# Kernel optimization log

Measured on AMD Instinct MI355X. Metric: run time of the kernel, lower is better.

## Reference

```python
import jax, jax.numpy as jnp
import numpy as np

D_NODE, D_PAIR, H = 512, 128, 16
HD = D_NODE // H  # head_dim = 32
B, N = 2, 1024


def _layernorm(x, gamma, beta, eps=1e-5):
    mu = jnp.mean(x, axis=-1, keepdims=True)
    var = jnp.var(x, axis=-1, keepdims=True)
    return (x - mu) * jax.lax.rsqrt(var + eps) * gamma + beta


def setup_inputs() -> dict:
    key = jax.random.key(0)
    ks = jax.random.split(key, 16)
    sc = 0.02
    inp = {
        's': jax.random.normal(ks[0], (B, N, D_NODE), jnp.float32),
        'z': jax.random.normal(ks[1], (B, N, N, D_PAIR), jnp.float32),
        'key_mask': jax.random.randint(ks[2], (B, N), 0, 2).astype(bool),
        'Wq': jax.random.normal(ks[3], (D_NODE, D_NODE), jnp.float32) * sc,
        'bq': jnp.zeros((D_NODE,), jnp.float32),
        'Wk': jax.random.normal(ks[4], (D_NODE, D_NODE), jnp.float32) * sc,
        'bk': jnp.zeros((D_NODE,), jnp.float32),
        'Wv': jax.random.normal(ks[5], (D_NODE, D_NODE), jnp.float32) * sc,
        'bv': jnp.zeros((D_NODE,), jnp.float32),
        'Wb': jax.random.normal(ks[6], (D_PAIR, H), jnp.float32) * sc,
        'bb': jnp.zeros((H,), jnp.float32),
        'Wg': jax.random.normal(ks[7], (D_NODE, D_NODE), jnp.float32) * sc,
        'bg': jnp.zeros((D_NODE,), jnp.float32),
        'Wo': jax.random.normal(ks[8], (D_NODE, D_NODE), jnp.float32) * sc,
        'bo': jnp.zeros((D_NODE,), jnp.float32),
        'gamma': jnp.ones((D_NODE,), jnp.float32),
        'beta': jnp.zeros((D_NODE,), jnp.float32),
    }
    return inp


def reference(s, z, key_mask, Wq, bq, Wk, bk, Wv, bv, Wb, bb, Wg, bg, Wo, bo, gamma, beta):
    b, n, _ = s.shape
    sn = _layernorm(s, gamma, beta)
    q = (sn @ Wq + bq).reshape(b, n, H, HD)
    k = (sn @ Wk + bk).reshape(b, n, H, HD)
    v = (sn @ Wv + bv).reshape(b, n, H, HD)
    # scores: [B, N(query), N(key), H]
    scores = jnp.einsum('bnhd,bmhd->bnmh', q, k) / np.sqrt(HD).astype(np.float32)
    scores = scores + (z @ Wb + bb)  # additive pair bias
    # mask keys (dim 2); True = masked out
    scores = jnp.where(key_mask[:, None, :, None], -jnp.inf, scores)
    attn = jax.nn.softmax(scores, axis=2)
    attn = jnp.nan_to_num(attn, nan=0.0)
    out = jnp.einsum('bnmh,bmhd->bnhd', attn, v).reshape(b, n, D_NODE)
    gate = jax.nn.sigmoid(sn @ Wg + bg)
    return gate * (out @ Wo + bo)
```

## Files before the change

### kernel.cpp

```cpp
#include <hip/hip_runtime.h>
#include <hip/hip_fp16.h>

typedef __attribute__((ext_vector_type(8))) _Float16 f16x8;
typedef __attribute__((ext_vector_type(8))) unsigned short u16x8;
typedef __attribute__((ext_vector_type(4))) float f32x4;

#define DEV __device__ __forceinline__

DEV unsigned short f2h(float f) {
  _Float16 h = (_Float16)f;
  return __builtin_bit_cast(unsigned short, h);
}
DEV float h2f(unsigned short u) {
  return (float)__builtin_bit_cast(_Float16, u);
}
DEV unsigned pk(float lo, float hi) {
  return (unsigned)f2h(lo) | ((unsigned)f2h(hi) << 16);
}

__global__ __launch_bounds__(256) void k_mask(const unsigned* __restrict__ raw,
                                              int* __restrict__ canon) {
  __shared__ int s_gt1, s_f32;
  int t = threadIdx.x;
  if (t == 0) { s_gt1 = 0; s_f32 = 0; }
  __syncthreads();
  int gt1 = 0, fv = 0;
  for (int i = t; i < 512; i += 256) {
    unsigned v = raw[i];
    if (v == 0x3F800000u) fv = 1;
    else if (v > 1u) gt1 = 1;
  }
  if (gt1) s_gt1 = 1;
  if (fv)  s_f32 = 1;
  __syncthreads();
  int mode = s_gt1 ? 1 : (s_f32 ? 2 : 0);
  for (int i = t; i < 2048; i += 256) {
    int v;
    if (mode == 1)      v = ((const unsigned char*)raw)[i] ? 1 : 0;
    else if (mode == 2) v = (((const float*)raw)[i] != 0.f) ? 1 : 0;
    else                v = raw[i] ? 1 : 0;
    canon[i] = v;
  }
}

__global__ __launch_bounds__(64) void k_ln(const float* __restrict__ s,
                                           const float* __restrict__ gamma,
                                           const float* __restrict__ beta,
                                           unsigned short* __restrict__ sn) {
  int row = blockIdx.x, l = threadIdx.x;
  const float* sr = s + (size_t)row * 512 + l * 8;
  float4 x0 = *(const float4*)sr, x1 = *(const float4*)(sr + 4);
  float sum = x0.x + x0.y + x0.z + x0.w + x1.x + x1.y + x1.z + x1.w;
  float sq  = x0.x*x0.x + x0.y*x0.y + x0.z*x0.z + x0.w*x0.w
            + x1.x*x1.x + x1.y*x1.y + x1.z*x1.z + x1.w*x1.w;
#pragma unroll
  for (int off = 32; off >= 1; off >>= 1) {
    sum += __shfl_xor(sum, off);
    sq  += __shfl_xor(sq, off);
  }
  float mu = sum * (1.f / 512.f);
  float rstd = rsqrtf(sq * (1.f / 512.f) - mu * mu + 1e-5f);
  float4 g0 = *(const float4*)(gamma + l * 8), g1 = *(const float4*)(gamma + l * 8 + 4);
  float4 b0 = *(const float4*)(beta + l * 8),  b1 = *(const float4*)(beta + l * 8 + 4);
  u16x8 o;
  o[0] = f2h((x0.x - mu) * rstd * g0.x + b0.x);
  o[1] = f2h((x0.y - mu) * rstd * g0.y + b0.y);
  o[2] = f2h((x0.z - mu) * rstd * g0.z + b0.z);
  o[3] = f2h((x0.w - mu) * rstd * g0.w + b0.w);
  o[4] = f2h((x1.x - mu) * rstd * g1.x + b1.x);
  o[5] = f2h((x1.y - mu) * rstd * g1.y + b1.y);
  o[6] = f2h((x1.z - mu) * rstd * g1.z + b1.z);
  o[7] = f2h((x1.w - mu) * rstd * g1.w + b1.w);
  *(u16x8*)(sn + (size_t)row * 512 + l * 8) = o;
}

DEV void gemm_body(const unsigned short* __restrict__ A,
                   const float* __restrict__ W,
                   const float* __restrict__ bvec,
                   void* __restrict__ outp,
                   const float* __restrict__ gate,
                   int mode, int ct, int rt) {
  int t = threadIdx.x, l = t & 63, w = t >> 6;
  __shared__ unsigned short As[128 * 40];
  __shared__ unsigned short Bs[128 * 40];
  f32x4 acc[4][4];
#pragma unroll
  for (int mt = 0; mt < 4; ++mt)
#pragma unroll
    for (int nt = 0; nt < 4; ++nt) acc[mt][nt] = (f32x4){0.f, 0.f, 0.f, 0.f};

  int arow = t >> 1, akc = (t & 1) * 16;
  int bkk = t >> 3, bc0 = (t & 7) * 16;
  int wr = w >> 1, wc = w & 1;

  for (int k0 = 0; k0 < 512; k0 += 32) {
    const u16x8* ap = (const u16x8*)(A + (size_t)(rt * 128 + arow) * 512 + k0 + akc);
    u16x8 a0 = ap[0], a1 = ap[1];
    *(u16x8*)(&As[arow * 40 + akc]) = a0;
    *(u16x8*)(&As[arow * 40 + akc + 8]) = a1;
    const float* wp = W + (size_t)(k0 + bkk) * 512 + ct * 128 + bc0;
#pragma unroll
    for (int i = 0; i < 4; ++i) {
      float4 f = *(const float4*)(wp + i * 4);
      Bs[(bc0 + i * 4 + 0) * 40 + bkk] = f2h(f.x);
      Bs[(bc0 + i * 4 + 1) * 40 + bkk] = f2h(f.y);
      Bs[(bc0 + i * 4 + 2) * 40 + bkk] = f2h(f.z);
      Bs[(bc0 + i * 4 + 3) * 40 + bkk] = f2h(f.w);
    }
    __syncthreads();
    f16x8 af[4], bf[4];
#pragma unroll
    for (int mt = 0; mt < 4; ++mt)
      af[mt] = *(const f16x8*)(&As[(wr * 64 + mt * 16 + (l & 15)) * 40 + (l >> 4) * 8]);
#pragma unroll
    for (int nt = 0; nt < 4; ++nt)
      bf[nt] = *(const f16x8*)(&Bs[(wc * 64 + nt * 16 + (l & 15)) * 40 + (l >> 4) * 8]);
#pragma unroll
    for (int mt = 0; mt < 4; ++mt)
#pragma unroll
      for (int nt = 0; nt < 4; ++nt)
        acc[mt][nt] = __builtin_amdgcn_mfma_f32_16x16x32_f16(af[mt], bf[nt], acc[mt][nt], 0, 0, 0);
    __syncthreads();
  }

#pragma unroll
  for (int mt = 0; mt < 4; ++mt)
#pragma unroll
    for (int nt = 0; nt < 4; ++nt) {
      int col = ct * 128 + wc * 64 + nt * 16 + (l & 15);
      float bv = bvec[col];
#pragma unroll
      for (int i = 0; i < 4; ++i) {
        int row = rt * 128 + wr * 64 + mt * 16 + (l >> 4) * 4 + i;
        float val = acc[mt][nt][i] + bv;
        int bb_ = row >> 10, n = row & 1023, hh = col >> 5, d = col & 31;
        if (mode == 0) {
          ((unsigned short*)outp)[(size_t)row * 512 + col] = f2h(val);
        } else if (mode == 1) {
          ((unsigned short*)outp)[(((size_t)bb_ * 16 + hh) * 1024 + n) * 32 + d] = f2h(val);
        } else if (mode == 2) {
          ((unsigned short*)outp)[(((size_t)bb_ * 16 + hh) * 32 + d) * 1024 + n] = f2h(val);
        } else if (mode == 3) {
          ((float*)outp)[(size_t)row * 512 + col] = 1.f / (1.f + __expf(-val));
        } else {
          ((float*)outp)[(size_t)row * 512 + col] = gate[(size_t)row * 512 + col] * val;
        }
      }
    }
}

__global__ __launch_bounds__(256) void k_qkvg(const unsigned short* __restrict__ A,
                                              const float* __restrict__ W0, const float* __restrict__ W1,
                                              const float* __restrict__ W2, const float* __restrict__ W3,
                                              const float* __restrict__ b0, const float* __restrict__ b1,
                                              const float* __restrict__ b2, const float* __restrict__ b3,
                                              void* o0, void* o1, void* o2, void* o3) {
  int mode = blockIdx.z;
  const float* W = (mode == 0) ? W0 : (mode == 1) ? W1 : (mode == 2) ? W2 : W3;
  const float* bv = (mode == 0) ? b0 : (mode == 1) ? b1 : (mode == 2) ? b2 : b3;
  void* o = (mode == 0) ? o0 : (mode == 1) ? o1 : (mode == 2) ? o2 : o3;
  gemm_body(A, W, bv, o, nullptr, mode, blockIdx.x, blockIdx.y);
}

__global__ __launch_bounds__(256) void k_gemm_out(const unsigned short* __restrict__ A,
                                                  const float* __restrict__ W,
                                                  const float* __restrict__ bvec,
                                                  float* __restrict__ outp,
                                                  const float* __restrict__ gate) {
  gemm_body(A, W, bvec, outp, gate, 4, blockIdx.x, blockIdx.y);
}

__global__ __launch_bounds__(256, 4) void k_bias(const float* __restrict__ z,
                                                 const float* __restrict__ Wb,
                                                 const float* __restrict__ bbp,
                                                 const int* __restrict__ maskc,
                                                 unsigned short* __restrict__ bias) {
  int bid = blockIdx.x;
  int slab = bid >> 1, half = bid & 1;
  int b = slab >> 10;
  int t = threadIdx.x, l = t & 63, w = t >> 6;
  int lane15 = l & 15, g = l >> 4;

  __shared__ float lds_[4][2048];
  float* wlds = lds_[w];

  f16x8 wf[4];
#pragma unroll
  for (int ks = 0; ks < 4; ++ks)
#pragma unroll
    for (int j = 0; j < 8; ++j)
      wf[ks][j] = (_Float16)Wb[(ks * 32 + g * 8 + j) * 16 + lane15];
  float bbh = bbp[lane15];

  const char* zb = (const char*)(z + ((size_t)slab * 1024 + half * 512 + (size_t)w * 128) * 128);
  unsigned short* ob = bias + ((size_t)slab * 16 + lane15) * 1024;
  const int* mrow = maskc + b * 1024;

  float4 rbuf[8];
#pragma unroll
  for (int i = 0; i < 8; ++i)
    rbuf[i] = *(const float4*)(zb + i * 1024 + l * 16);
#pragma unroll
  for (int i = 0; i < 8; ++i) {
    int lin = i * 1024 + l * 16;
    int off = lin ^ (((lin >> 9) & 7) << 4);
    *(float4*)((char*)wlds + off) = rbuf[i];
  }

  for (int t8 = 0; t8 < 8; ++t8) {
    if (t8 < 7) {
      const char* tb = zb + (t8 + 1) * 8192;
#pragma unroll
      for (int i = 0; i < 8; ++i)
        rbuf[i] = *(const float4*)(tb + i * 1024 + l * 16);
    }
    f32x4 acc = (f32x4){0.f, 0.f, 0.f, 0.f};
#pragma unroll
    for (int ks = 0; ks < 4; ++ks) {
      int linA = lane15 * 512 + ks * 128 + g * 32;
      int swz = ((lane15 & 7) << 4);
      float4 z0 = *(const float4*)((const char*)wlds + (linA ^ swz));
      float4 z1 = *(const float4*)((const char*)wlds + ((linA + 16) ^ swz));
      f16x8 af;
      af[0] = (_Float16)z0.x; af[1] = (_Float16)z0.y;
      af[2] = (_Float16)z0.z; af[3] = (_Float16)z0.w;
      af[4] = (_Float16)z1.x; af[5] = (_Float16)z1.y;
      af[6] = (_Float16)z1.z; af[7] = (_Float16)z1.w;
      acc = __builtin_amdgcn_mfma_f32_16x16x32_f16(af, wf[ks], acc, 0, 0, 0);
    }
    int mabs = half * 512 + w * 128 + t8 * 16 + 4 * g;
    int4 mk = *(const int4*)(mrow + mabs);
    ushort4 o4;
    o4.x = mk.x ? 0xFBFFu : f2h(acc[0] + bbh);
    o4.y = mk.y ? 0xFBFFu : f2h(acc[1] + bbh);
    o4.z = mk.z ? 0xFBFFu : f2h(acc[2] + bbh);
    o4.w = mk.w ? 0xFBFFu : f2h(acc[3] + bbh);
    *(ushort4*)(ob + mabs) = o4;
    if (t8 < 7) {
#pragma unroll
      for (int i = 0; i < 8; ++i) {
        int lin = i * 1024 + l * 16;
        int off = lin ^ (((lin >> 9) & 7) << 4);
        *(float4*)((char*)wlds + off) = rbuf[i];
      }
    }
  }
}

__global__ __launch_bounds__(512, 4) void k_attn(const unsigned short* __restrict__ qbuf,
                                                 const unsigned short* __restrict__ kbuf,
                                                 const unsigned short* __restrict__ vbuf,
                                                 const unsigned short* __restrict__ bias,
                                                 unsigned short* __restrict__ aout) {
  int qt = blockIdx.x, h = blockIdx.y, b = blockIdx.z;
  int t = threadIdx.x, l = t & 63, w = t >> 6;
  int qs = w & 3, half = w >> 2;
  int q0 = (qt * 4 + qs) * 16;
  int lane15 = l & 15, g = l >> 4;
  int bh = b * 16 + h;
  const float RS = 0.17677669529663687f;

  __shared__ float red_m[4][64];
  __shared__ float red_l[4][64];
  __shared__ f32x4 red_a1[4][64];
  __shared__ f32x4 red_a2[4][64];

  f16x8 qf = *(const f16x8*)(qbuf + ((size_t)(b * 1024 + q0 + lane15)) * 512 + h * 32 + g * 8);

  const unsigned short* kb_ = kbuf + (size_t)bh * 1024 * 32 + (size_t)half * 512 * 32;
  const unsigned short* vb_ = vbuf + (size_t)bh * 32 * 1024 + half * 512;
  const unsigned short* brow = bias + ((size_t)(b * 1024 + q0 + lane15) * 16 + h) * 1024 + half * 512;

  float m_run = -3.0e38f, lsum = 0.f;
  f32x4 acc1 = (f32x4){0.f, 0.f, 0.f, 0.f};
  f32x4 acc2 = (f32x4){0.f, 0.f, 0.f, 0.f};

  for (int c = 0; c < 16; ++c) {
    int m0 = c * 32;
    f16x8 kf1 = *(const f16x8*)(kb_ + (size_t)(m0 + lane15) * 32 + g * 8);
    f16x8 kf2 = *(const f16x8*)(kb_ + (size_t)(m0 + 16 + lane15) * 32 + g * 8);
    f32x4 zero = (f32x4){0.f, 0.f, 0.f, 0.f};
    f32x4 c1 = __builtin_amdgcn_mfma_f32_16x16x32_f16(kf1, qf, zero, 0, 0, 0);
    f32x4 c2 = __builtin_amdgcn_mfma_f32_16x16x32_f16(kf2, qf, zero, 0, 0, 0);
    ushort4 bv1 = *(const ushort4*)(brow + m0 + 4 * g);
    ushort4 bv2 = *(const ushort4*)(brow + m0 + 16 + 4 * g);
    float s1[4], s2[4];
    s1[0] = c1[0] * RS + h2f(bv1.x); s1[1] = c1[1] * RS + h2f(bv1.y);
    s1[2] = c1[2] * RS + h2f(bv1.z); s1[3] = c1[3] * RS + h2f(bv1.w);
    s2[0] = c2[0] * RS + h2f(bv2.x); s2[1] = c2[1] * RS + h2f(bv2.y);
    s2[2] = c2[2] * RS + h2f(bv2.z); s2[3] = c2[3] * RS + h2f(bv2.w);
    float cm = fmaxf(fmaxf(fmaxf(s1[0], s1[1]), fmaxf(s1[2], s1[3])),
                     fmaxf(fmaxf(s2[0], s2[1]), fmaxf(s2[2], s2[3])));
    cm = fmaxf(cm, __shfl_xor(cm, 16));
    cm = fmaxf(cm, __shfl_xor(cm, 32));
    float mn = fmaxf(m_run, cm);
    float corr = __expf(m_run - mn);
    m_run = mn;
    float p1[4], p2[4], csum = 0.f;
#pragma unroll
    for (int i = 0; i < 4; ++i) { p1[i] = __expf(s1[i] - mn); csum += p1[i]; }
#pragma unroll
    for (int i = 0; i < 4; ++i) { p2[i] = __expf(s2[i] - mn); csum += p2[i]; }
    lsum = lsum * corr + csum;
#pragma unroll
    for (int i = 0; i < 4; ++i) { acc1[i] *= corr; acc2[i] *= corr; }
    unsigned a0 = pk(p1[0], p1[1]), a1 = pk(p1[2], p1[3]);
    unsigned b0 = pk(p2[0], p2[1]), b1 = pk(p2[2], p2[3]);
    int s0 = ((g & 1) << 5) + lane15, s1l = s0 + 16;
    unsigned wA0 = (unsigned)__shfl((int)a0, s0);
    unsigned wA1 = (unsigned)__shfl((int)a1, s0);
    unsigned wA2 = (unsigned)__shfl((int)a0, s1l);
    unsigned wA3 = (unsigned)__shfl((int)a1, s1l);
    unsigned wB0 = (unsigned)__shfl((int)b0, s0);
    unsigned wB1 = (unsigned)__shfl((int)b1, s0);
    unsigned wB2 = (unsigned)__shfl((int)b0, s1l);
    unsigned wB3 = (unsigned)__shfl((int)b1, s1l);
    bool hi = (l & 32) != 0;
    union { unsigned u[4]; f16x8 v; } pu;
    pu.u[0] = hi ? wB0 : wA0;
    pu.u[1] = hi ? wB1 : wA1;
    pu.u[2] = hi ? wB2 : wA2;
    pu.u[3] = hi ? wB3 : wA3;
    f16x8 vf1 = *(const f16x8*)(vb_ + (size_t)lane15 * 1024 + m0 + 8 * g);
    f16x8 vf2 = *(const f16x8*)(vb_ + (size_t)(16 + lane15) * 1024 + m0 + 8 * g);
    acc1 = __builtin_amdgcn_mfma_f32_16x16x32_f16(vf1, pu.v, acc1, 0, 0, 0);
    acc2 = __builtin_amdgcn_mfma_f32_16x16x32_f16(vf2, pu.v, acc2, 0, 0, 0);
  }

  lsum += __shfl_xor(lsum, 16);
  lsum += __shfl_xor(lsum, 32);

  if (half) {
    red_m[qs][l] = m_run;
    red_l[qs][l] = lsum;
    red_a1[qs][l] = acc1;
    red_a2[qs][l] = acc2;
  }
  __syncthreads();
  if (!half) {
    float pm = red_m[qs][l], plv = red_l[qs][l];
    f32x4 pa1 = red_a1[qs][l], pa2 = red_a2[qs][l];
    float mm = fmaxf(m_run, pm);
    float c1s = __expf(m_run - mm), c2s = __expf(pm - mm);
    float lt = lsum * c1s + plv * c2s;
    float inv = (mm > -30000.f && lt > 0.f) ? 1.f / lt : 0.f;
    unsigned short* orow = aout + ((size_t)(b * 1024 + q0 + lane15)) * 512 + h * 32;
    ushort4 o1, o2;
    o1.x = f2h((acc1[0] * c1s + pa1[0] * c2s) * inv);
    o1.y = f2h((acc1[1] * c1s + pa1[1] * c2s) * inv);
    o1.z = f2h((acc1[2] * c1s + pa1[2] * c2s) * inv);
    o1.w = f2h((acc1[3] * c1s + pa1[3] * c2s) * inv);
    o2.x = f2h((acc2[0] * c1s + pa2[0] * c2s) * inv);
    o2.y = f2h((acc2[1] * c1s + pa2[1] * c2s) * inv);
    o2.z = f2h((acc2[2] * c1s + pa2[2] * c2s) * inv);
    o2.w = f2h((acc2[3] * c1s + pa2[3] * c2s) * inv);
    *(ushort4*)(orow + 4 * g) = o1;
    *(ushort4*)(orow + 16 + 4 * g) = o2;
  }
}

extern "C" void kernel_launch(void* const* d_in, const int* in_sizes, int n_in,
                              void* d_out, int out_size, void* d_ws, size_t ws_size,
                              hipStream_t stream) {
  (void)in_sizes; (void)n_in; (void)out_size; (void)ws_size;
  const float* s     = (const float*)d_in[0];
  const float* z     = (const float*)d_in[1];
  const unsigned* km = (const unsigned*)d_in[2];
  const float* Wq = (const float*)d_in[3];
  const float* bq = (const float*)d_in[4];
  const float* Wk = (const float*)d_in[5];
  const float* bk = (const float*)d_in[6];
  const float* Wv = (const float*)d_in[7];
  const float* bv = (const float*)d_in[8];
  const float* Wb = (const float*)d_in[9];
  const float* bb = (const float*)d_in[10];
  const float* Wg = (const float*)d_in[11];
  const float* bg = (const float*)d_in[12];
  const float* Wo = (const float*)d_in[13];
  const float* bo = (const float*)d_in[14];
  const float* gamma = (const float*)d_in[15];
  const float* beta  = (const float*)d_in[16];

  char* ws = (char*)d_ws;
  unsigned short* sn    = (unsigned short*)(ws);
  unsigned short* qbuf  = (unsigned short*)(ws + (2ull << 20));
  unsigned short* kbuf  = (unsigned short*)(ws + (4ull << 20));
  unsigned short* vbuf  = (unsigned short*)(ws + (6ull << 20));
  float*          gate  = (float*)(ws + (8ull << 20));
  unsigned short* aout  = (unsigned short*)(ws + (12ull << 20));
  unsigned short* bias  = (unsigned short*)(ws + (14ull << 20));
  int*            maskc = (int*)(ws + (78ull << 20));

  hipLaunchKernelGGL(k_mask, dim3(1), dim3(256), 0, stream, km, maskc);
  hipLaunchKernelGGL(k_ln, dim3(2048), dim3(64), 0, stream, s, gamma, beta, sn);
  hipLaunchKernelGGL(k_qkvg, dim3(4, 16, 4), dim3(256), 0, stream, sn,
                     Wq, Wk, Wv, Wg, bq, bk, bv, bg,
                     (void*)qbuf, (void*)kbuf, (void*)vbuf, (void*)gate);
  hipLaunchKernelGGL(k_bias, dim3(4096), dim3(256), 0, stream, z, Wb, bb, maskc, bias);
  hipLaunchKernelGGL(k_attn, dim3(16, 16, 2), dim3(512), 0, stream,
                     qbuf, kbuf, vbuf, bias, aout);
  hipLaunchKernelGGL(k_gemm_out, dim3(4, 16), dim3(256), 0, stream, aout, Wo, bo,
                     (float*)d_out, gate);
}
```

Before: 358.2 us.

## Pre-transpose weights to fp16, use register-direct GEMMs, prefetch attention chunks

Adds a prep kernel that transposes and converts all five weight matrices to fp16 once per call and folds the mask canonicalisation into it. The projection GEMMs then load A and transposed-W fragments straight from global memory into registers with one-step prefetch. They use half-width column tiles and twice the grid, and no longer stage through LDS or call __syncthreads. The attention loop now prefetches the next chunk's K, V and bias fragments while the current chunk is being computed. The trade-off is an extra kernel, more register pressure, and uncoalesced-ish direct global fragment loads that rely on cache reuse.

```diff
diff --git a/kernel.cpp b/kernel.cpp
--- a/kernel.cpp
+++ b/kernel.cpp
@@ -18,28 +18,49 @@
   return (unsigned)f2h(lo) | ((unsigned)f2h(hi) << 16);
 }
 
-__global__ __launch_bounds__(256) void k_mask(const unsigned* __restrict__ raw,
-                                              int* __restrict__ canon) {
-  __shared__ int s_gt1, s_f32;
+__global__ __launch_bounds__(256) void k_prep(const float* __restrict__ W0, const float* __restrict__ W1,
+                                              const float* __restrict__ W2, const float* __restrict__ W3,
+                                              const float* __restrict__ W4,
+                                              unsigned short* __restrict__ T0, unsigned short* __restrict__ T1,
+                                              unsigned short* __restrict__ T2, unsigned short* __restrict__ T3,
+                                              unsigned short* __restrict__ T4,
+                                              const unsigned* __restrict__ raw, int* __restrict__ canon) {
+  int mat = blockIdx.y;
+  const float* W = (mat == 0) ? W0 : (mat == 1) ? W1 : (mat == 2) ? W2 : (mat == 3) ? W3 : W4;
+  unsigned short* T = (mat == 0) ? T0 : (mat == 1) ? T1 : (mat == 2) ? T2 : (mat == 3) ? T3 : T4;
+  int tx = blockIdx.x & 7, ty = blockIdx.x >> 3;
+  __shared__ float tile[64][65];
   int t = threadIdx.x;
-  if (t == 0) { s_gt1 = 0; s_f32 = 0; }
+  int r = t >> 6, c = t & 63;
+#pragma unroll
+  for (int i = 0; i < 16; ++i)
+    tile[r + i * 4][c] = W[(size_t)(ty * 64 + r + i * 4) * 512 + tx * 64 + c];
   __syncthreads();
-  int gt1 = 0, fv = 0;
-  for (int i = t; i < 512; i += 256) {
-    unsigned v = raw[i];
-    if (v == 0x3F800000u) fv = 1;
-    else if (v > 1u) gt1 = 1;
-  }
-  if (gt1) s_gt1 = 1;
-  if (fv)  s_f32 = 1;
-  __syncthreads();
-  int mode = s_gt1 ? 1 : (s_f32 ? 2 : 0);
-  for (int i = t; i < 2048; i += 256) {
-    int v;
-    if (mode == 1)      v = ((const unsigned char*)raw)[i] ? 1 : 0;
-    else if (mode == 2) v = (((const float*)raw)[i] != 0.f) ? 1 : 0;
-    else                v = raw[i] ? 1 : 0;
-    canon[i] = v;
+#pragma unroll
+  for (int i = 0; i < 16; ++i)
+    T[(size_t)(tx * 64 + r + i * 4) * 512 + ty * 64 + c] = f2h(tile[c][r + i * 4]);
+
+  if (mat == 0 && blockIdx.x == 0) {
+    __shared__ int s_gt1, s_f32;
+    if (t == 0) { s_gt1 = 0; s_f32 = 0; }
+    __syncthreads();
+    int gt1 = 0, fv = 0;
+    for (int i = t; i < 512; i += 256) {
+      unsigned v = raw[i];
+      if (v == 0x3F800000u) fv = 1;
+      else if (v > 1u) gt1 = 1;
+    }
+    if (gt1) s_gt1 = 1;
+    if (fv)  s_f32 = 1;
+    __syncthreads();
+    int mode = s_gt1 ? 1 : (s_f32 ? 2 : 0);
+    for (int i = t; i < 2048; i += 256) {
+      int v;
+      if (mode == 1)      v = ((const unsigned char*)raw)[i] ? 1 : 0;
+      else if (mode == 2) v = (((const float*)raw)[i] != 0.f) ? 1 : 0;
+      else                v = raw[i] ? 1 : 0;
+      canon[i] = v;
+    }
   }
 }
 
@@ -74,64 +95,69 @@
   *(u16x8*)(sn + (size_t)row * 512 + l * 8) = o;
 }
 
-DEV void gemm_body(const unsigned short* __restrict__ A,
-                   const float* __restrict__ W,
-                   const float* __restrict__ bvec,
-                   void* __restrict__ outp,
-                   const float* __restrict__ gate,
-                   int mode, int ct, int rt) {
+DEV void gemm_direct(const unsigned short* __restrict__ A,
+                     const unsigned short* __restrict__ Wt,
+                     const float* __restrict__ bvec,
+                     void* __restrict__ outp,
+                     const float* __restrict__ gate,
+                     int mode, int ct, int rt) {
   int t = threadIdx.x, l = t & 63, w = t >> 6;
-  __shared__ unsigned short As[128 * 40];
-  __shared__ unsigned short Bs[128 * 40];
-  f32x4 acc[4][4];
+  int lane15 = l & 15, g = l >> 4;
+  int wr = w >> 1, wc = w & 1;
+  const unsigned short* ap[4];
+  const unsigned short* bp[2];
 #pragma unroll
   for (int mt = 0; mt < 4; ++mt)
-#pragma unroll
-    for (int nt = 0; nt < 4; ++nt) acc[mt][nt] = (f32x4){0.f, 0.f, 0.f, 0.f};
-
-  int arow = t >> 1, akc = (t & 1) * 16;
-  int bkk = t >> 3, bc0 = (t & 7) * 16;
-  int wr = w >> 1, wc = w & 1;
-
-  for (int k0 = 0; k0 < 512; k0 += 32) {
-    const u16x8* ap = (const u16x8*)(A + (size_t)(rt * 128 + arow) * 512 + k0 + akc);
-    u16x8 a0 = ap[0], a1 = ap[1];
-    *(u16x8*)(&As[arow * 40 + akc]) = a0;
-    *(u16x8*)(&As[arow * 40 + akc + 8]) = a1;
-    const float* wp = W + (size_t)(k0 + bkk) * 512 + ct * 128 + bc0;
-#pragma unroll
-    for (int i = 0; i < 4; ++i) {
-      float4 f = *(const float4*)(wp + i * 4);
-      Bs[(bc0 + i * 4 + 0) * 40 + bkk] = f2h(f.x);
-      Bs[(bc0 + i * 4 + 1) * 40 + bkk] = f2h(f.y);
-      Bs[(bc0 + i * 4 + 2) * 40 + bkk] = f2h(f.z);
-      Bs[(bc0 + i * 4 + 3) * 40 + bkk] = f2h(f.w);
-    }
-    __syncthreads();
-    f16x8 af[4], bf[4];
+    ap[mt] = A + (size_t)(rt * 128 + wr * 64 + mt * 16 + lane15) * 512 + g * 8;
+#pragma unroll
+  for (int nt = 0; nt < 2; ++nt)
+    bp[nt] = Wt + (size_t)(ct * 64 + wc * 32 + nt * 16 + lane15) * 512 + g * 8;
+
+  f32x4 acc[4][2];
+#pragma unroll
+  for (int mt = 0; mt < 4; ++mt)
+#pragma unroll
+    for (int nt = 0; nt < 2; ++nt) acc[mt][nt] = (f32x4){0.f, 0.f, 0.f, 0.f};
+
+  f16x8 af[4], bf[2];
+#pragma unroll
+  for (int mt = 0; mt < 4; ++mt) af[mt] = *(const f16x8*)ap[mt];
+#pragma unroll
+  for (int nt = 0; nt < 2; ++nt) bf[nt] = *(const f16x8*)bp[nt];
+
+  for (int ks = 0; ks < 16; ++ks) {
+    f16x8 an[4], bn[2];
+    if (ks < 15) {
+#pragma unroll
+      for (int mt = 0; mt < 4; ++mt) an[mt] = *(const f16x8*)(ap[mt] + (ks + 1) * 32);
+#pragma unroll
+      for (int nt = 0; nt < 2; ++nt) bn[nt] = *(const f16x8*)(bp[nt] + (ks + 1) * 32);
+    } else {
+#pragma unroll
+      for (int mt = 0; mt < 4; ++mt) an[mt] = af[mt];
+#pragma unroll
+      for (int nt = 0; nt < 2; ++nt) bn[nt] = bf[nt];
+    }
 #pragma unroll
     for (int mt = 0; mt < 4; ++mt)
-      af[mt] = *(const f16x8*)(&As[(wr * 64 + mt * 16 + (l & 15)) * 40 + (l >> 4) * 8]);
-#pragma unroll
-    for (int nt = 0; nt < 4; ++nt)
-      bf[nt] = *(const f16x8*)(&Bs[(wc * 64 + nt * 16 + (l & 15)) * 40 + (l >> 4) * 8]);
-#pragma unroll
-    for (int mt = 0; mt < 4; ++mt)
-#pragma unroll
-      for (int nt = 0; nt < 4; ++nt)
+#pragma unroll
+      for (int nt = 0; nt < 2; ++nt)
         acc[mt][nt] = __builtin_amdgcn_mfma_f32_16x16x32_f16(af[mt], bf[nt], acc[mt][nt], 0, 0, 0);
-    __syncthreads();
+#pragma unroll
+    for (int mt = 0; mt < 4; ++mt) af[mt] = an[mt];
+#pragma unroll
+    for (int nt = 0; nt < 2; ++nt) bf[nt] = bn[nt];
   }
 
 #pragma unroll
   for (int mt = 0; mt < 4; ++mt)
 #pragma unroll
-    for (int nt = 0; nt < 4; ++nt) {
-      int col = ct * 128 + wc * 64 + nt * 16 + (l & 15);
+    for (int nt = 0; nt < 2; ++nt) {
+      int col = ct * 64 + wc * 32 + nt * 16 + lane15;
       float bv = bvec[col];
 #pragma unroll
       for (int i = 0; i < 4; ++i) {
-        int row = rt * 128 + wr * 64 + mt * 16 + (l >> 4) * 4 + i;
+        int row = rt * 128 + wr * 64 + mt * 16 + g * 4 + i;
         float val = acc[mt][nt][i] + bv;
         int bb_ = row >> 10, n = row & 1023, hh = col >> 5, d = col & 31;
         if (mode == 0) {
@@ -150,24 +176,24 @@
 }
 
 __global__ __launch_bounds__(256) void k_qkvg(const unsigned short* __restrict__ A,
-                                              const float* __restrict__ W0, const float* __restrict__ W1,
-                                              const float* __restrict__ W2, const float* __restrict__ W3,
+                                              const unsigned short* __restrict__ T0, const unsigned short* __restrict__ T1,
+                                              const unsigned short* __restrict__ T2, const unsigned short* __restrict__ T3,
                                               const float* __restrict__ b0, const float* __restrict__ b1,
                                               const float* __restrict__ b2, const float* __restrict__ b3,
                                               void* o0, void* o1, void* o2, void* o3) {
   int mode = blockIdx.z;
-  const float* W = (mode == 0) ? W0 : (mode == 1) ? W1 : (mode == 2) ? W2 : W3;
+  const unsigned short* Wt = (mode == 0) ? T0 : (mode == 1) ? T1 : (mode == 2) ? T2 : T3;
   const float* bv = (mode == 0) ? b0 : (mode == 1) ? b1 : (mode == 2) ? b2 : b3;
   void* o = (mode == 0) ? o0 : (mode == 1) ? o1 : (mode == 2) ? o2 : o3;
-  gemm_body(A, W, bv, o, nullptr, mode, blockIdx.x, blockIdx.y);
+  gemm_direct(A, Wt, bv, o, nullptr, mode, blockIdx.x, blockIdx.y);
 }
 
 __global__ __launch_bounds__(256) void k_gemm_out(const unsigned short* __restrict__ A,
-                                                  const float* __restrict__ W,
+                                                  const unsigned short* __restrict__ Wt,
                                                   const float* __restrict__ bvec,
                                                   float* __restrict__ outp,
                                                   const float* __restrict__ gate) {
-  gemm_body(A, W, bvec, outp, gate, 4, blockIdx.x, blockIdx.y);
+  gemm_direct(A, Wt, bvec, outp, gate, 4, blockIdx.x, blockIdx.y);
 }
 
 __global__ __launch_bounds__(256, 4) void k_bias(const float* __restrict__ z,
@@ -245,6 +271,23 @@
       }
     }
   }
+}
+
+struct Pf {
+  f16x8 kf1, kf2, vf1, vf2;
+  ushort4 bv1, bv2;
+};
+DEV Pf ldchunk(const unsigned short* kb_, const unsigned short* vb_,
+               const unsigned short* brow, int lane15, int g, int c) {
+  Pf p;
+  int m0 = c * 32;
+  p.kf1 = *(const f16x8*)(kb_ + (size_t)(m0 + lane15) * 32 + g * 8);
+  p.kf2 = *(const f16x8*)(kb_ + (size_t)(m0 + 16 + lane15) * 32 + g * 8);
+  p.bv1 = *(const ushort4*)(brow + m0 + 4 * g);
+  p.bv2 = *(const ushort4*)(brow + m0 + 16 + 4 * g);
+  p.vf1 = *(const f16x8*)(vb_ + (size_t)lane15 * 1024 + m0 + 8 * g);
+  p.vf2 = *(const f16x8*)(vb_ + (size_t)(16 + lane15) * 1024 + m0 + 8 * g);
+  return p;
 }
 
 __global__ __launch_bounds__(512, 4) void k_attn(const unsigned short* __restrict__ qbuf,
@@ -275,20 +318,20 @@
   f32x4 acc1 = (f32x4){0.f, 0.f, 0.f, 0.f};
   f32x4 acc2 = (f32x4){0.f, 0.f, 0.f, 0.f};
 
+  Pf cur = ldchunk(kb_, vb_, brow, lane15, g, 0);
+
   for (int c = 0; c < 16; ++c) {
-    int m0 = c * 32;
-    f16x8 kf1 = *(const f16x8*)(kb_ + (size_t)(m0 + lane15) * 32 + g * 8);
-    f16x8 kf2 = *(const f16x8*)(kb_ + (size_t)(m0 + 16 + lane15) * 32 + g * 8);
+    Pf nxt = cur;
+    if (c < 15) nxt = ldchunk(kb_, vb_, brow, lane15, g, c + 1);
+
     f32x4 zero = (f32x4){0.f, 0.f, 0.f, 0.f};
-    f32x4 c1 = __builtin_amdgcn_mfma_f32_16x16x32_f16(kf1, qf, zero, 0, 0, 0);
-    f32x4 c2 = __builtin_amdgcn_mfma_f32_16x16x32_f16(kf2, qf, zero, 0, 0, 0);
-    ushort4 bv1 = *(const ushort4*)(brow + m0 + 4 * g);
-    ushort4 bv2 = *(const ushort4*)(brow + m0 + 16 + 4 * g);
+    f32x4 c1 = __builtin_amdgcn_mfma_f32_16x16x32_f16(cur.kf1, qf, zero, 0, 0, 0);
+    f32x4 c2 = __builtin_amdgcn_mfma_f32_16x16x32_f16(cur.kf2, qf, zero, 0, 0, 0);
     float s1[4], s2[4];
-    s1[0] = c1[0] * RS + h2f(bv1.x); s1[1] = c1[1] * RS + h2f(bv1.y);
-    s1[2] = c1[2] * RS + h2f(bv1.z); s1[3] = c1[3] * RS + h2f(bv1.w);
-    s2[0] = c2[0] * RS + h2f(bv2.x); s2[1] = c2[1] * RS + h2f(bv2.y);
-    s2[2] = c2[2] * RS + h2f(bv2.z); s2[3] = c2[3] * RS + h2f(bv2.w);
+    s1[0] = c1[0] * RS + h2f(cur.bv1.x); s1[1] = c1[1] * RS + h2f(cur.bv1.y);
+    s1[2] = c1[2] * RS + h2f(cur.bv1.z); s1[3] = c1[3] * RS + h2f(cur.bv1.w);
+    s2[0] = c2[0] * RS + h2f(cur.bv2.x); s2[1] = c2[1] * RS + h2f(cur.bv2.y);
+    s2[2] = c2[2] * RS + h2f(cur.bv2.z); s2[3] = c2[3] * RS + h2f(cur.bv2.w);
     float cm = fmaxf(fmaxf(fmaxf(s1[0], s1[1]), fmaxf(s1[2], s1[3])),
                      fmaxf(fmaxf(s2[0], s2[1]), fmaxf(s2[2], s2[3])));
     cm = fmaxf(cm, __shfl_xor(cm, 16));
@@ -321,10 +364,9 @@
     pu.u[1] = hi ? wB1 : wA1;
     pu.u[2] = hi ? wB2 : wA2;
     pu.u[3] = hi ? wB3 : wA3;
-    f16x8 vf1 = *(const f16x8*)(vb_ + (size_t)lane15 * 1024 + m0 + 8 * g);
-    f16x8 vf2 = *(const f16x8*)(vb_ + (size_t)(16 + lane15) * 1024 + m0 + 8 * g);
-    acc1 = __builtin_amdgcn_mfma_f32_16x16x32_f16(vf1, pu.v, acc1, 0, 0, 0);
-    acc2 = __builtin_amdgcn_mfma_f32_16x16x32_f16(vf2, pu.v, acc2, 0, 0, 0);
+    acc1 = __builtin_amdgcn_mfma_f32_16x16x32_f16(cur.vf1, pu.v, acc1, 0, 0, 0);
+    acc2 = __builtin_amdgcn_mfma_f32_16x16x32_f16(cur.vf2, pu.v, acc2, 0, 0, 0);
+    cur = nxt;
   }
 
   lsum += __shfl_xor(lsum, 16);
@@ -390,15 +432,21 @@
   unsigned short* aout  = (unsigned short*)(ws + (12ull << 20));
   unsigned short* bias  = (unsigned short*)(ws + (14ull << 20));
   int*            maskc = (int*)(ws + (78ull << 20));
-
-  hipLaunchKernelGGL(k_mask, dim3(1), dim3(256), 0, stream, km, maskc);
+  unsigned short* wtq   = (unsigned short*)(ws + (80ull << 20));
+  unsigned short* wtk   = (unsigned short*)(ws + (80ull << 20) + (512u << 10));
+  unsigned short* wtv   = (unsigned short*)(ws + (80ull << 20) + (1024u << 10));
+  unsigned short* wtg   = (unsigned short*)(ws + (80ull << 20) + (1536u << 10));
+  unsigned short* wto   = (unsigned short*)(ws + (80ull << 20) + (2048u << 10));
+
+  hipLaunchKernelGGL(k_prep, dim3(64, 5), dim3(256), 0, stream,
+                     Wq, Wk, Wv, Wg, Wo, wtq, wtk, wtv, wtg, wto, km, maskc);
   hipLaunchKernelGGL(k_ln, dim3(2048), dim3(64), 0, stream, s, gamma, beta, sn);
-  hipLaunchKernelGGL(k_qkvg, dim3(4, 16, 4), dim3(256), 0, stream, sn,
-                     Wq, Wk, Wv, Wg, bq, bk, bv, bg,
+  hipLaunchKernelGGL(k_qkvg, dim3(8, 16, 4), dim3(256), 0, stream, sn,
+                     wtq, wtk, wtv, wtg, bq, bk, bv, bg,
                      (void*)qbuf, (void*)kbuf, (void*)vbuf, (void*)gate);
   hipLaunchKernelGGL(k_bias, dim3(4096), dim3(256), 0, stream, z, Wb, bb, maskc, bias);
   hipLaunchKernelGGL(k_attn, dim3(16, 16, 2), dim3(512), 0, stream,
                      qbuf, kbuf, vbuf, bias, aout);
-  hipLaunchKernelGGL(k_gemm_out, dim3(4, 16), dim3(256), 0, stream, aout, Wo, bo,
+  hipLaunchKernelGGL(k_gemm_out, dim3(8, 16), dim3(256), 0, stream, aout, wto, bo,
                      (float*)d_out, gate);
 }
```

Result: faster. 345.1 us (-3.7%).
